# Optimization experiments

Hardware: AMD Instinct MI355X
Metric: run time of the kernel (lower is better)

The kernel has to match this reference:

```python
import jax, jax.numpy as jnp
import numpy as np

TOP_K = 2


def setup_inputs() -> dict:
    key = jax.random.key(0)
    k_x, k_g, k_w1, k_w2, k_w3 = jax.random.split(key, 5)
    B, S, D, H, E = 2, 512, 1024, 512, 8
    x = jax.random.normal(k_x, (B, S, D), dtype=jnp.float32)
    gate_w = jax.random.normal(k_g, (D, E), dtype=jnp.float32) * (D ** -0.5)
    w1 = jax.random.normal(k_w1, (E, D, H), dtype=jnp.float32) * 0.02  # gate proj
    w2 = jax.random.normal(k_w2, (E, H, D), dtype=jnp.float32) * 0.02  # down proj
    w3 = jax.random.normal(k_w3, (E, D, H), dtype=jnp.float32) * 0.02  # up proj
    return {"x": x, "gate_w": gate_w, "w1": w1, "w2": w2, "w3": w3}


def reference(x, gate_w, w1, w2, w3):
    # Token-choice top-k MoE with grouped SwiGLU experts, no shared expert.
    # Equivalent to torchtune MoE: gather routed tokens, scale by top-k router
    # score, run per-expert FFN, scatter-add back. Since each expert's FFN has
    # no bias (FFN(0) == 0), the dispatch/grouped-GEMM/combine is expressed
    # densely as sum_e FFN_e(scale[:, e] * x), which is mathematically identical.
    B, S, D = x.shape
    E = gate_w.shape[1]
    xf = x.reshape(B * S, D)                      # [T, D]
    T = B * S

    logits = xf @ gate_w                          # [T, E]
    scores = jax.nn.softmax(logits, axis=-1)
    top_scores, top_idx = jax.lax.top_k(scores, TOP_K)  # [T, k]

    # scale[t, e] = router score if expert e selected for token t, else 0
    scale = jnp.zeros((T, E), dtype=x.dtype).at[
        jnp.arange(T)[:, None], top_idx
    ].set(top_scores)

    xs = scale.T[:, :, None] * xf[None, :, :]     # [E, T, D] scaled routed input
    h = jax.nn.silu(jnp.einsum('etd,edh->eth', xs, w1)) \
        * jnp.einsum('etd,edh->eth', xs, w3)      # [E, T, H]
    y = jnp.einsum('eth,ehd->etd', h, w2)         # [E, T, D]
    out = y.sum(axis=0)                           # combine (scatter-add equiv)
    return out.reshape(B, S, D)
```

## Files before the change

### kernel.cpp

```cpp
#include <hip/hip_runtime.h>
#include <hip/hip_bf16.h>
#include <cstddef>

#define T_TOK 1024
#define D_DIM 1024
#define H_DIM 512
#define E_EXP 8
#define P_CAP 2560
#define MAX_MT (P_CAP / 64)
#define LDA 72

typedef __attribute__((ext_vector_type(4))) float    float4_t;
typedef __attribute__((ext_vector_type(4))) short    short4_t;
typedef __attribute__((ext_vector_type(8))) short    short8_t;
typedef __attribute__((ext_vector_type(4))) unsigned uint4_t;
typedef __attribute__((ext_vector_type(2))) unsigned uint2_t;

__device__ __forceinline__ short f2bf(float f) {
  union { float f; unsigned u; } v; v.f = f;
  unsigned u = v.u;
  u += 0x7FFFu + ((u >> 16) & 1u);
  return (short)(u >> 16);
}

__device__ __forceinline__ unsigned pkbf(float a, float b) {
  union { __hip_bfloat162 h; unsigned u; } v;
  v.h = __float22bfloat162_rn(make_float2(a, b));
  return v.u;
}

__global__ __launch_bounds__(256) void wconv_kernel(
    const float* __restrict__ src, short* __restrict__ dst,
    int K, int N, int ld_dst, int row_off, size_t src_es, size_t dst_es) {
  __shared__ float tile[64][68];
  const int e  = blockIdx.z;
  const int k0 = blockIdx.x * 64;
  const int n0 = blockIdx.y * 64;
  const int tid = threadIdx.x;
  const float* s = src + (size_t)e * src_es;
  const int kr = tid >> 4, nc = (tid & 15) * 4;
  #pragma unroll
  for (int p = 0; p < 4; ++p) {
    int k = p * 16 + kr;
    float4_t v = *(const float4_t*)(s + (size_t)(k0 + k) * N + n0 + nc);
    *(float4_t*)&tile[k][nc] = v;
  }
  __syncthreads();
  const int r8 = tid >> 3, c8 = tid & 7;
  short* d = dst + (size_t)e * dst_es;
  #pragma unroll
  for (int p = 0; p < 2; ++p) {
    int row = p * 32 + r8;
    uint4_t u;
    #pragma unroll
    for (int j = 0; j < 4; ++j)
      u[j] = pkbf(tile[c8 * 8 + 2 * j][row], tile[c8 * 8 + 2 * j + 1][row]);
    *(uint4_t*)(d + (size_t)(row_off + n0 + row) * ld_dst + k0 + c8 * 8) = u;
  }
}

__global__ __launch_bounds__(256) void router_kernel(
    const float* __restrict__ x, const float* __restrict__ gw,
    int* __restrict__ idx2, float* __restrict__ scale2) {
  const int wid  = threadIdx.x >> 6;
  const int lane = threadIdx.x & 63;
  const int t = blockIdx.x * 4 + wid;
  const float* xr = x + (size_t)t * D_DIM;
  float acc[E_EXP];
  #pragma unroll
  for (int e = 0; e < E_EXP; ++e) acc[e] = 0.f;
  for (int d = lane; d < D_DIM; d += 64) {
    float xv = xr[d];
    float4_t g0 = *(const float4_t*)(gw + d * E_EXP);
    float4_t g1 = *(const float4_t*)(gw + d * E_EXP + 4);
    acc[0] += xv * g0[0]; acc[1] += xv * g0[1];
    acc[2] += xv * g0[2]; acc[3] += xv * g0[3];
    acc[4] += xv * g1[0]; acc[5] += xv * g1[1];
    acc[6] += xv * g1[2]; acc[7] += xv * g1[3];
  }
  #pragma unroll
  for (int off = 32; off >= 1; off >>= 1) {
    #pragma unroll
    for (int e = 0; e < E_EXP; ++e) acc[e] += __shfl_down(acc[e], off, 64);
  }
  if (lane == 0) {
    float m = acc[0];
    #pragma unroll
    for (int e = 1; e < E_EXP; ++e) m = fmaxf(m, acc[e]);
    float p[E_EXP]; float s = 0.f;
    #pragma unroll
    for (int e = 0; e < E_EXP; ++e) { p[e] = __expf(acc[e] - m); s += p[e]; }
    float inv = 1.f / s;
    #pragma unroll
    for (int e = 0; e < E_EXP; ++e) p[e] *= inv;
    int i1 = 0;
    #pragma unroll
    for (int e = 1; e < E_EXP; ++e) if (p[e] > p[i1]) i1 = e;
    int i2 = (i1 == 0) ? 1 : 0;
    #pragma unroll
    for (int e = 0; e < E_EXP; ++e) {
      if (e == i1 || e == i2) continue;
      if (p[e] > p[i2]) i2 = e;
    }
    idx2[2 * t]     = i1;  scale2[2 * t]     = p[i1];
    idx2[2 * t + 1] = i2;  scale2[2 * t + 1] = p[i2];
  }
}

__global__ __launch_bounds__(256) void scan_kernel(
    const int* __restrict__ idx2, const float* __restrict__ scale2,
    int* __restrict__ pair_tok, float* __restrict__ pair_scale,
    int* __restrict__ meta) {
  __shared__ int cnt[E_EXP], base[E_EXP], cur[E_EXP];
  const int tid = threadIdx.x;
  if (tid < E_EXP) { cnt[tid] = 0; cur[tid] = 0; }
  for (int p = tid; p < P_CAP; p += 256) { pair_tok[p] = -1; pair_scale[p] = 0.f; }
  __syncthreads();
  for (int t = tid; t < T_TOK; t += 256) {
    atomicAdd(&cnt[idx2[2 * t]], 1);
    atomicAdd(&cnt[idx2[2 * t + 1]], 1);
  }
  __syncthreads();
  if (tid == 0) {
    int b = 0, g = 0;
    for (int e = 0; e < E_EXP; ++e) {
      base[e] = b;
      int al = (cnt[e] + 63) & ~63;
      for (int j = 0; j < al; j += 64) { meta[1 + g] = e; meta[41 + g] = b + j; ++g; }
      b += al;
    }
    meta[0] = g;
  }
  __syncthreads();
  for (int t = tid; t < T_TOK; t += 256) {
    #pragma unroll
    for (int s = 0; s < 2; ++s) {
      int e = idx2[2 * t + s];
      int p = base[e] + atomicAdd(&cur[e], 1);
      pair_tok[p] = t;
      pair_scale[p] = scale2[2 * t + s];
    }
  }
}

__global__ __launch_bounds__(256, 2) void gemm1_kernel(
    const float* __restrict__ x, const short* __restrict__ w13t,
    const int* __restrict__ pair_tok, const float* __restrict__ pair_scale,
    const int* __restrict__ meta, short* __restrict__ h) {
  __shared__ short As[64 * LDA], B1s[64 * LDA], B3s[64 * LDA];
  const int mt = blockIdx.y;
  if (mt >= meta[0]) return;
  const int e    = meta[1 + mt];
  const int row0 = meta[41 + mt];
  const int n0   = blockIdx.x * 64;
  const int tid = threadIdx.x, lane = tid & 63, wid = tid >> 6;
  const int wr = wid >> 1, wc = wid & 1;
  const int q = lane >> 4, ln = lane & 15;
  const short* bsrc = w13t + (size_t)e * D_DIM * (2 * H_DIM);

  const int ar = tid >> 2, ak = tid & 3;
  const int   tokr = pair_tok[row0 + ar];
  const float sc   = pair_scale[row0 + ar];
  const float* xrow = x + (size_t)(tokr < 0 ? 0 : tokr) * D_DIM + ak * 16;

  const int br = tid >> 3, bu = tid & 7;

  float4_t acc1[2][2], acc3[2][2];
  #pragma unroll
  for (int i = 0; i < 2; ++i)
    #pragma unroll
    for (int j = 0; j < 2; ++j) {
      acc1[i][j] = (float4_t){0.f, 0.f, 0.f, 0.f};
      acc3[i][j] = (float4_t){0.f, 0.f, 0.f, 0.f};
    }

  for (int k0 = 0; k0 < D_DIM; k0 += 64) {
    {
      float4_t v0 = *(const float4_t*)(xrow + k0);
      float4_t v1 = *(const float4_t*)(xrow + k0 + 4);
      float4_t v2 = *(const float4_t*)(xrow + k0 + 8);
      float4_t v3 = *(const float4_t*)(xrow + k0 + 12);
      uint4_t u0 = {pkbf(v0[0] * sc, v0[1] * sc), pkbf(v0[2] * sc, v0[3] * sc),
                    pkbf(v1[0] * sc, v1[1] * sc), pkbf(v1[2] * sc, v1[3] * sc)};
      uint4_t u1 = {pkbf(v2[0] * sc, v2[1] * sc), pkbf(v2[2] * sc, v2[3] * sc),
                    pkbf(v3[0] * sc, v3[1] * sc), pkbf(v3[2] * sc, v3[3] * sc)};
      *(uint4_t*)&As[ar * LDA + ak * 16]     = u0;
      *(uint4_t*)&As[ar * LDA + ak * 16 + 8] = u1;
    }
    #pragma unroll
    for (int p = 0; p < 2; ++p) {
      int row = p * 32 + br;
      uint4_t v1 = *(const uint4_t*)(bsrc + (size_t)(n0 + row) * D_DIM + k0 + bu * 8);
      uint4_t v3 = *(const uint4_t*)(bsrc + (size_t)(H_DIM + n0 + row) * D_DIM + k0 + bu * 8);
      *(uint4_t*)&B1s[row * LDA + bu * 8] = v1;
      *(uint4_t*)&B3s[row * LDA + bu * 8] = v3;
    }
    __syncthreads();

    short8_t af[2][2], b1f[2][2], b3f[2][2];
    #pragma unroll
    for (int i = 0; i < 2; ++i)
      #pragma unroll
      for (int kk = 0; kk < 2; ++kk)
        af[i][kk] = *(const short8_t*)&As[(wr * 32 + i * 16 + ln) * LDA + kk * 32 + q * 8];
    #pragma unroll
    for (int j = 0; j < 2; ++j)
      #pragma unroll
      for (int kk = 0; kk < 2; ++kk) {
        b1f[j][kk] = *(const short8_t*)&B1s[(wc * 32 + j * 16 + ln) * LDA + kk * 32 + q * 8];
        b3f[j][kk] = *(const short8_t*)&B3s[(wc * 32 + j * 16 + ln) * LDA + kk * 32 + q * 8];
      }
    #pragma unroll
    for (int i = 0; i < 2; ++i)
      #pragma unroll
      for (int j = 0; j < 2; ++j)
        #pragma unroll
        for (int kk = 0; kk < 2; ++kk) {
          acc1[i][j] = __builtin_amdgcn_mfma_f32_16x16x32_bf16(af[i][kk], b1f[j][kk], acc1[i][j], 0, 0, 0);
          acc3[i][j] = __builtin_amdgcn_mfma_f32_16x16x32_bf16(af[i][kk], b3f[j][kk], acc3[i][j], 0, 0, 0);
        }
    __syncthreads();
  }

  #pragma unroll
  for (int i = 0; i < 2; ++i) {
    int r_base = row0 + wr * 32 + i * 16 + q * 4;
    #pragma unroll
    for (int j = 0; j < 2; ++j) {
      int col = n0 + wc * 32 + j * 16 + ln;
      #pragma unroll
      for (int rr = 0; rr < 4; ++rr) {
        float c1 = acc1[i][j][rr];
        float c3 = acc3[i][j][rr];
        float sig = 1.f / (1.f + __expf(-c1));
        h[(size_t)(r_base + rr) * H_DIM + col] = f2bf(c1 * sig * c3);
      }
    }
  }
}

__global__ __launch_bounds__(256, 2) void gemm2_kernel(
    const short* __restrict__ h, const short* __restrict__ w2t,
    const int* __restrict__ pair_tok, const int* __restrict__ meta,
    float* __restrict__ out) {
  __shared__ short As[64 * LDA], Bs[64 * LDA];
  const int mt = blockIdx.y;
  if (mt >= meta[0]) return;
  const int e    = meta[1 + mt];
  const int row0 = meta[41 + mt];
  const int n0   = blockIdx.x * 64;
  const int tid = threadIdx.x, lane = tid & 63, wid = tid >> 6;
  const int wr = wid >> 1, wc = wid & 1;
  const int q = lane >> 4, ln = lane & 15;
  const short* bsrc = w2t + (size_t)e * D_DIM * H_DIM;

  const int ar = tid >> 2, ak = tid & 3;
  const short* hrow = h + (size_t)(row0 + ar) * H_DIM + ak * 16;
  const int br = tid >> 3, bu = tid & 7;

  float4_t acc[2][2];
  #pragma unroll
  for (int i = 0; i < 2; ++i)
    #pragma unroll
    for (int j = 0; j < 2; ++j) acc[i][j] = (float4_t){0.f, 0.f, 0.f, 0.f};

  for (int k0 = 0; k0 < H_DIM; k0 += 64) {
    {
      uint4_t u0 = *(const uint4_t*)(hrow + k0);
      uint4_t u1 = *(const uint4_t*)(hrow + k0 + 8);
      *(uint4_t*)&As[ar * LDA + ak * 16]     = u0;
      *(uint4_t*)&As[ar * LDA + ak * 16 + 8] = u1;
    }
    #pragma unroll
    for (int p = 0; p < 2; ++p) {
      int row = p * 32 + br;
      uint4_t v = *(const uint4_t*)(bsrc + (size_t)(n0 + row) * H_DIM + k0 + bu * 8);
      *(uint4_t*)&Bs[row * LDA + bu * 8] = v;
    }
    __syncthreads();

    short8_t af[2][2], bf[2][2];
    #pragma unroll
    for (int i = 0; i < 2; ++i)
      #pragma unroll
      for (int kk = 0; kk < 2; ++kk)
        af[i][kk] = *(const short8_t*)&As[(wr * 32 + i * 16 + ln) * LDA + kk * 32 + q * 8];
    #pragma unroll
    for (int j = 0; j < 2; ++j)
      #pragma unroll
      for (int kk = 0; kk < 2; ++kk)
        bf[j][kk] = *(const short8_t*)&Bs[(wc * 32 + j * 16 + ln) * LDA + kk * 32 + q * 8];
    #pragma unroll
    for (int i = 0; i < 2; ++i)
      #pragma unroll
      for (int j = 0; j < 2; ++j)
        #pragma unroll
        for (int kk = 0; kk < 2; ++kk)
          acc[i][j] = __builtin_amdgcn_mfma_f32_16x16x32_bf16(af[i][kk], bf[j][kk], acc[i][j], 0, 0, 0);
    __syncthreads();
  }

  #pragma unroll
  for (int i = 0; i < 2; ++i) {
    int r_base = row0 + wr * 32 + i * 16 + q * 4;
    #pragma unroll
    for (int rr = 0; rr < 4; ++rr) {
      int tok = pair_tok[r_base + rr];
      if (tok < 0) continue;
      float* orow = out + (size_t)tok * D_DIM;
      #pragma unroll
      for (int j = 0; j < 2; ++j) {
        int col = n0 + wc * 32 + j * 16 + ln;
        atomicAdd(orow + col, acc[i][j][rr]);
      }
    }
  }
}

extern "C" void kernel_launch(void* const* d_in, const int* in_sizes, int n_in,
                              void* d_out, int out_size, void* d_ws, size_t ws_size,
                              hipStream_t stream) {
  const float* x  = (const float*)d_in[0];
  const float* gw = (const float*)d_in[1];
  const float* w1 = (const float*)d_in[2];
  const float* w2 = (const float*)d_in[3];
  const float* w3 = (const float*)d_in[4];
  float* out = (float*)d_out;

  char* ws = (char*)d_ws;
  int*   idx2    = (int*)  (ws);
  float* scale2  = (float*)(ws + 8192);
  int*   ptok    = (int*)  (ws + 16384);
  float* pscale  = (float*)(ws + 32768);
  int*   meta    = (int*)  (ws + 49152);
  short* h       = (short*)(ws + 65536);
  short* w13t    = (short*)(ws + 65536 + (size_t)P_CAP * H_DIM * 2);
  short* w2t     = w13t + (size_t)E_EXP * D_DIM * 2 * H_DIM;

  wconv_kernel<<<dim3(16, 8, E_EXP), dim3(256), 0, stream>>>(
      w1, w13t, D_DIM, H_DIM, D_DIM, 0,     (size_t)D_DIM * H_DIM, (size_t)D_DIM * 2 * H_DIM);
  wconv_kernel<<<dim3(16, 8, E_EXP), dim3(256), 0, stream>>>(
      w3, w13t, D_DIM, H_DIM, D_DIM, H_DIM, (size_t)D_DIM * H_DIM, (size_t)D_DIM * 2 * H_DIM);
  wconv_kernel<<<dim3(8, 16, E_EXP), dim3(256), 0, stream>>>(
      w2, w2t, H_DIM, D_DIM, H_DIM, 0,      (size_t)H_DIM * D_DIM, (size_t)D_DIM * H_DIM);

  router_kernel<<<dim3(T_TOK / 4), dim3(256), 0, stream>>>(x, gw, idx2, scale2);
  scan_kernel<<<dim3(1), dim3(256), 0, stream>>>(idx2, scale2, ptok, pscale, meta);

  gemm1_kernel<<<dim3(H_DIM / 64, MAX_MT), dim3(256), 0, stream>>>(
      x, w13t, ptok, pscale, meta, h);

  hipMemsetAsync(out, 0, (size_t)T_TOK * D_DIM * sizeof(float), stream);
  gemm2_kernel<<<dim3(D_DIM / 64, MAX_MT), dim3(256), 0, stream>>>(
      h, w2t, ptok, meta, out);
}
```

Measured before the change: 158.3 us.

## Double-buffer GEMM tiles, pre-convert routed inputs, merge weight conversion launches

Both expert GEMMs now use register-staged double-buffered shared-memory tiles, so global loads for the next K step overlap the MFMA work on the current one. A new xsconv kernel gathers, scales and converts routed tokens to bf16 once, so gemm1 no longer converts fp32 per tile. Gemm1's N tile is halved to 32 to launch more blocks. The three weight-conversion launches are merged into one grid, and the workspace layout is reorganised. The cost is an extra kernel plus a bf16 xs buffer write and read, and more shared memory per block.

```diff
diff --git a/kernel.cpp b/kernel.cpp
--- a/kernel.cpp
+++ b/kernel.cpp
@@ -11,10 +11,8 @@
 #define LDA 72
 
 typedef __attribute__((ext_vector_type(4))) float    float4_t;
-typedef __attribute__((ext_vector_type(4))) short    short4_t;
 typedef __attribute__((ext_vector_type(8))) short    short8_t;
 typedef __attribute__((ext_vector_type(4))) unsigned uint4_t;
-typedef __attribute__((ext_vector_type(2))) unsigned uint2_t;
 
 __device__ __forceinline__ short f2bf(float f) {
   union { float f; unsigned u; } v; v.f = f;
@@ -30,24 +28,36 @@
 }
 
 __global__ __launch_bounds__(256) void wconv_kernel(
-    const float* __restrict__ src, short* __restrict__ dst,
-    int K, int N, int ld_dst, int row_off, size_t src_es, size_t dst_es) {
+    const float* __restrict__ w1, const float* __restrict__ w3,
+    const float* __restrict__ w2, short* __restrict__ w13t,
+    short* __restrict__ w2t) {
   __shared__ float tile[64][68];
-  const int e  = blockIdx.z;
-  const int k0 = blockIdx.x * 64;
-  const int n0 = blockIdx.y * 64;
+  const int z = blockIdx.z;
+  const float* src; short* dst; int N, ldd, row_off; size_t ses, des;
+  if (z < 16) {
+    if (blockIdx.y >= 8) return;
+    int which = z >> 3, e = z & 7;
+    src = (which ? w3 : w1) + (size_t)e * D_DIM * H_DIM;
+    dst = w13t + (size_t)e * D_DIM * (2 * H_DIM);
+    N = H_DIM; ldd = D_DIM; row_off = which ? H_DIM : 0;
+  } else {
+    if (blockIdx.x >= 8) return;
+    int e = z - 16;
+    src = w2 + (size_t)e * H_DIM * D_DIM;
+    dst = w2t + (size_t)e * D_DIM * H_DIM;
+    N = D_DIM; ldd = H_DIM; row_off = 0;
+  }
+  const int k0 = blockIdx.x * 64, n0 = blockIdx.y * 64;
   const int tid = threadIdx.x;
-  const float* s = src + (size_t)e * src_es;
   const int kr = tid >> 4, nc = (tid & 15) * 4;
   #pragma unroll
   for (int p = 0; p < 4; ++p) {
     int k = p * 16 + kr;
-    float4_t v = *(const float4_t*)(s + (size_t)(k0 + k) * N + n0 + nc);
+    float4_t v = *(const float4_t*)(src + (size_t)(k0 + k) * N + n0 + nc);
     *(float4_t*)&tile[k][nc] = v;
   }
   __syncthreads();
   const int r8 = tid >> 3, c8 = tid & 7;
-  short* d = dst + (size_t)e * dst_es;
   #pragma unroll
   for (int p = 0; p < 2; ++p) {
     int row = p * 32 + r8;
@@ -55,7 +65,7 @@
     #pragma unroll
     for (int j = 0; j < 4; ++j)
       u[j] = pkbf(tile[c8 * 8 + 2 * j][row], tile[c8 * 8 + 2 * j + 1][row]);
-    *(uint4_t*)(d + (size_t)(row_off + n0 + row) * ld_dst + k0 + c8 * 8) = u;
+    *(uint4_t*)(dst + (size_t)(row_off + n0 + row) * ldd + k0 + c8 * 8) = u;
   }
 }
 
@@ -143,98 +153,111 @@
   }
 }
 
+__global__ __launch_bounds__(256) void xsconv_kernel(
+    const float* __restrict__ x, const int* __restrict__ pair_tok,
+    const float* __restrict__ pair_scale, short* __restrict__ xs) {
+  const int row = blockIdx.x * 8 + (threadIdx.x >> 5);
+  const int seg = (threadIdx.x & 31) * 32;
+  const int tok = pair_tok[row];
+  const float sc = pair_scale[row];
+  const float* src = x + (size_t)(tok < 0 ? 0 : tok) * D_DIM + seg;
+  short* dst = xs + (size_t)row * D_DIM + seg;
+  #pragma unroll
+  for (int p = 0; p < 2; ++p) {
+    float4_t v0 = *(const float4_t*)(src + p * 16);
+    float4_t v1 = *(const float4_t*)(src + p * 16 + 4);
+    float4_t v2 = *(const float4_t*)(src + p * 16 + 8);
+    float4_t v3 = *(const float4_t*)(src + p * 16 + 12);
+    uint4_t u0 = {pkbf(v0[0] * sc, v0[1] * sc), pkbf(v0[2] * sc, v0[3] * sc),
+                  pkbf(v1[0] * sc, v1[1] * sc), pkbf(v1[2] * sc, v1[3] * sc)};
+    uint4_t u1 = {pkbf(v2[0] * sc, v2[1] * sc), pkbf(v2[2] * sc, v2[3] * sc),
+                  pkbf(v3[0] * sc, v3[1] * sc), pkbf(v3[2] * sc, v3[3] * sc)};
+    *(uint4_t*)(dst + p * 16)     = u0;
+    *(uint4_t*)(dst + p * 16 + 8) = u1;
+  }
+}
+
 __global__ __launch_bounds__(256, 2) void gemm1_kernel(
-    const float* __restrict__ x, const short* __restrict__ w13t,
-    const int* __restrict__ pair_tok, const float* __restrict__ pair_scale,
+    const short* __restrict__ xs, const short* __restrict__ w13t,
     const int* __restrict__ meta, short* __restrict__ h) {
-  __shared__ short As[64 * LDA], B1s[64 * LDA], B3s[64 * LDA];
+  __shared__ short As[2][64 * LDA];
+  __shared__ short B1s[2][32 * LDA];
+  __shared__ short B3s[2][32 * LDA];
   const int mt = blockIdx.y;
   if (mt >= meta[0]) return;
   const int e    = meta[1 + mt];
   const int row0 = meta[41 + mt];
-  const int n0   = blockIdx.x * 64;
+  const int n0   = blockIdx.x * 32;
   const int tid = threadIdx.x, lane = tid & 63, wid = tid >> 6;
   const int wr = wid >> 1, wc = wid & 1;
   const int q = lane >> 4, ln = lane & 15;
   const short* bsrc = w13t + (size_t)e * D_DIM * (2 * H_DIM);
 
-  const int ar = tid >> 2, ak = tid & 3;
-  const int   tokr = pair_tok[row0 + ar];
-  const float sc   = pair_scale[row0 + ar];
-  const float* xrow = x + (size_t)(tokr < 0 ? 0 : tokr) * D_DIM + ak * 16;
-
-  const int br = tid >> 3, bu = tid & 7;
-
-  float4_t acc1[2][2], acc3[2][2];
-  #pragma unroll
-  for (int i = 0; i < 2; ++i)
-    #pragma unroll
-    for (int j = 0; j < 2; ++j) {
-      acc1[i][j] = (float4_t){0.f, 0.f, 0.f, 0.f};
-      acc3[i][j] = (float4_t){0.f, 0.f, 0.f, 0.f};
-    }
-
-  for (int k0 = 0; k0 < D_DIM; k0 += 64) {
-    {
-      float4_t v0 = *(const float4_t*)(xrow + k0);
-      float4_t v1 = *(const float4_t*)(xrow + k0 + 4);
-      float4_t v2 = *(const float4_t*)(xrow + k0 + 8);
-      float4_t v3 = *(const float4_t*)(xrow + k0 + 12);
-      uint4_t u0 = {pkbf(v0[0] * sc, v0[1] * sc), pkbf(v0[2] * sc, v0[3] * sc),
-                    pkbf(v1[0] * sc, v1[1] * sc), pkbf(v1[2] * sc, v1[3] * sc)};
-      uint4_t u1 = {pkbf(v2[0] * sc, v2[1] * sc), pkbf(v2[2] * sc, v2[3] * sc),
-                    pkbf(v3[0] * sc, v3[1] * sc), pkbf(v3[2] * sc, v3[3] * sc)};
-      *(uint4_t*)&As[ar * LDA + ak * 16]     = u0;
-      *(uint4_t*)&As[ar * LDA + ak * 16 + 8] = u1;
-    }
-    #pragma unroll
-    for (int p = 0; p < 2; ++p) {
-      int row = p * 32 + br;
-      uint4_t v1 = *(const uint4_t*)(bsrc + (size_t)(n0 + row) * D_DIM + k0 + bu * 8);
-      uint4_t v3 = *(const uint4_t*)(bsrc + (size_t)(H_DIM + n0 + row) * D_DIM + k0 + bu * 8);
-      *(uint4_t*)&B1s[row * LDA + bu * 8] = v1;
-      *(uint4_t*)&B3s[row * LDA + bu * 8] = v3;
-    }
-    __syncthreads();
-
-    short8_t af[2][2], b1f[2][2], b3f[2][2];
+  const int ar = tid >> 2, ak = (tid & 3) * 16;
+  const short* arow = xs + (size_t)(row0 + ar) * D_DIM + ak;
+  const int br = tid >> 3, bu = (tid & 7) * 8;
+  const short* b1p = bsrc + (size_t)(n0 + br) * D_DIM + bu;
+  const short* b3p = bsrc + (size_t)(H_DIM + n0 + br) * D_DIM + bu;
+
+  float4_t acc1[2], acc3[2];
+  acc1[0] = acc1[1] = acc3[0] = acc3[1] = (float4_t){0.f, 0.f, 0.f, 0.f};
+
+  uint4_t va0 = *(const uint4_t*)(arow);
+  uint4_t va1 = *(const uint4_t*)(arow + 8);
+  uint4_t vb1 = *(const uint4_t*)(b1p);
+  uint4_t vb3 = *(const uint4_t*)(b3p);
+  *(uint4_t*)&As [0][ar * LDA + ak] = va0;
+  *(uint4_t*)&As [0][ar * LDA + ak + 8] = va1;
+  *(uint4_t*)&B1s[0][br * LDA + bu] = vb1;
+  *(uint4_t*)&B3s[0][br * LDA + bu] = vb3;
+  __syncthreads();
+
+  for (int k = 0; k < 16; ++k) {
+    const int cur = k & 1, nxt = cur ^ 1;
+    if (k < 15) {
+      int k0 = (k + 1) * 64;
+      va0 = *(const uint4_t*)(arow + k0);
+      va1 = *(const uint4_t*)(arow + k0 + 8);
+      vb1 = *(const uint4_t*)(b1p + k0);
+      vb3 = *(const uint4_t*)(b3p + k0);
+    }
+    short8_t af[2][2], b1f[2], b3f[2];
     #pragma unroll
     for (int i = 0; i < 2; ++i)
       #pragma unroll
       for (int kk = 0; kk < 2; ++kk)
-        af[i][kk] = *(const short8_t*)&As[(wr * 32 + i * 16 + ln) * LDA + kk * 32 + q * 8];
-    #pragma unroll
-    for (int j = 0; j < 2; ++j)
+        af[i][kk] = *(const short8_t*)&As[cur][(wr * 32 + i * 16 + ln) * LDA + kk * 32 + q * 8];
+    #pragma unroll
+    for (int kk = 0; kk < 2; ++kk) {
+      b1f[kk] = *(const short8_t*)&B1s[cur][(wc * 16 + ln) * LDA + kk * 32 + q * 8];
+      b3f[kk] = *(const short8_t*)&B3s[cur][(wc * 16 + ln) * LDA + kk * 32 + q * 8];
+    }
+    #pragma unroll
+    for (int i = 0; i < 2; ++i)
       #pragma unroll
       for (int kk = 0; kk < 2; ++kk) {
-        b1f[j][kk] = *(const short8_t*)&B1s[(wc * 32 + j * 16 + ln) * LDA + kk * 32 + q * 8];
-        b3f[j][kk] = *(const short8_t*)&B3s[(wc * 32 + j * 16 + ln) * LDA + kk * 32 + q * 8];
+        acc1[i] = __builtin_amdgcn_mfma_f32_16x16x32_bf16(af[i][kk], b1f[kk], acc1[i], 0, 0, 0);
+        acc3[i] = __builtin_amdgcn_mfma_f32_16x16x32_bf16(af[i][kk], b3f[kk], acc3[i], 0, 0, 0);
       }
-    #pragma unroll
-    for (int i = 0; i < 2; ++i)
-      #pragma unroll
-      for (int j = 0; j < 2; ++j)
-        #pragma unroll
-        for (int kk = 0; kk < 2; ++kk) {
-          acc1[i][j] = __builtin_amdgcn_mfma_f32_16x16x32_bf16(af[i][kk], b1f[j][kk], acc1[i][j], 0, 0, 0);
-          acc3[i][j] = __builtin_amdgcn_mfma_f32_16x16x32_bf16(af[i][kk], b3f[j][kk], acc3[i][j], 0, 0, 0);
-        }
+    if (k < 15) {
+      *(uint4_t*)&As [nxt][ar * LDA + ak] = va0;
+      *(uint4_t*)&As [nxt][ar * LDA + ak + 8] = va1;
+      *(uint4_t*)&B1s[nxt][br * LDA + bu] = vb1;
+      *(uint4_t*)&B3s[nxt][br * LDA + bu] = vb3;
+    }
     __syncthreads();
   }
 
   #pragma unroll
   for (int i = 0; i < 2; ++i) {
     int r_base = row0 + wr * 32 + i * 16 + q * 4;
-    #pragma unroll
-    for (int j = 0; j < 2; ++j) {
-      int col = n0 + wc * 32 + j * 16 + ln;
-      #pragma unroll
-      for (int rr = 0; rr < 4; ++rr) {
-        float c1 = acc1[i][j][rr];
-        float c3 = acc3[i][j][rr];
-        float sig = 1.f / (1.f + __expf(-c1));
-        h[(size_t)(r_base + rr) * H_DIM + col] = f2bf(c1 * sig * c3);
-      }
+    int col = n0 + wc * 16 + ln;
+    #pragma unroll
+    for (int rr = 0; rr < 4; ++rr) {
+      float c1 = acc1[i][rr];
+      float c3 = acc3[i][rr];
+      float sig = 1.f / (1.f + __expf(-c1));
+      h[(size_t)(r_base + rr) * H_DIM + col] = f2bf(c1 * sig * c3);
     }
   }
 }
@@ -243,7 +266,8 @@
     const short* __restrict__ h, const short* __restrict__ w2t,
     const int* __restrict__ pair_tok, const int* __restrict__ meta,
     float* __restrict__ out) {
-  __shared__ short As[64 * LDA], Bs[64 * LDA];
+  __shared__ short As[2][64 * LDA];
+  __shared__ short Bs[2][64 * LDA];
   const int mt = blockIdx.y;
   if (mt >= meta[0]) return;
   const int e    = meta[1 + mt];
@@ -254,9 +278,9 @@
   const int q = lane >> 4, ln = lane & 15;
   const short* bsrc = w2t + (size_t)e * D_DIM * H_DIM;
 
-  const int ar = tid >> 2, ak = tid & 3;
-  const short* hrow = h + (size_t)(row0 + ar) * H_DIM + ak * 16;
-  const int br = tid >> 3, bu = tid & 7;
+  const int ar = tid >> 2, ak = (tid & 3) * 16;
+  const short* arow = h + (size_t)(row0 + ar) * H_DIM + ak;
+  const short* brow = bsrc + (size_t)(n0 + ar) * H_DIM + ak;
 
   float4_t acc[2][2];
   #pragma unroll
@@ -264,32 +288,33 @@
     #pragma unroll
     for (int j = 0; j < 2; ++j) acc[i][j] = (float4_t){0.f, 0.f, 0.f, 0.f};
 
-  for (int k0 = 0; k0 < H_DIM; k0 += 64) {
-    {
-      uint4_t u0 = *(const uint4_t*)(hrow + k0);
-      uint4_t u1 = *(const uint4_t*)(hrow + k0 + 8);
-      *(uint4_t*)&As[ar * LDA + ak * 16]     = u0;
-      *(uint4_t*)&As[ar * LDA + ak * 16 + 8] = u1;
-    }
-    #pragma unroll
-    for (int p = 0; p < 2; ++p) {
-      int row = p * 32 + br;
-      uint4_t v = *(const uint4_t*)(bsrc + (size_t)(n0 + row) * H_DIM + k0 + bu * 8);
-      *(uint4_t*)&Bs[row * LDA + bu * 8] = v;
-    }
-    __syncthreads();
-
+  uint4_t va0 = *(const uint4_t*)(arow);
+  uint4_t va1 = *(const uint4_t*)(arow + 8);
+  uint4_t vb0 = *(const uint4_t*)(brow);
+  uint4_t vb1 = *(const uint4_t*)(brow + 8);
+  *(uint4_t*)&As[0][ar * LDA + ak] = va0;
+  *(uint4_t*)&As[0][ar * LDA + ak + 8] = va1;
+  *(uint4_t*)&Bs[0][ar * LDA + ak] = vb0;
+  *(uint4_t*)&Bs[0][ar * LDA + ak + 8] = vb1;
+  __syncthreads();
+
+  for (int k = 0; k < 8; ++k) {
+    const int cur = k & 1, nxt = cur ^ 1;
+    if (k < 7) {
+      int k0 = (k + 1) * 64;
+      va0 = *(const uint4_t*)(arow + k0);
+      va1 = *(const uint4_t*)(arow + k0 + 8);
+      vb0 = *(const uint4_t*)(brow + k0);
+      vb1 = *(const uint4_t*)(brow + k0 + 8);
+    }
     short8_t af[2][2], bf[2][2];
     #pragma unroll
     for (int i = 0; i < 2; ++i)
       #pragma unroll
-      for (int kk = 0; kk < 2; ++kk)
-        af[i][kk] = *(const short8_t*)&As[(wr * 32 + i * 16 + ln) * LDA + kk * 32 + q * 8];
-    #pragma unroll
-    for (int j = 0; j < 2; ++j)
-      #pragma unroll
-      for (int kk = 0; kk < 2; ++kk)
-        bf[j][kk] = *(const short8_t*)&Bs[(wc * 32 + j * 16 + ln) * LDA + kk * 32 + q * 8];
+      for (int kk = 0; kk < 2; ++kk) {
+        af[i][kk] = *(const short8_t*)&As[cur][(wr * 32 + i * 16 + ln) * LDA + kk * 32 + q * 8];
+        bf[i][kk] = *(const short8_t*)&Bs[cur][(wc * 32 + i * 16 + ln) * LDA + kk * 32 + q * 8];
+      }
     #pragma unroll
     for (int i = 0; i < 2; ++i)
       #pragma unroll
@@ -297,6 +322,12 @@
         #pragma unroll
         for (int kk = 0; kk < 2; ++kk)
           acc[i][j] = __builtin_amdgcn_mfma_f32_16x16x32_bf16(af[i][kk], bf[j][kk], acc[i][j], 0, 0, 0);
+    if (k < 7) {
+      *(uint4_t*)&As[nxt][ar * LDA + ak] = va0;
+      *(uint4_t*)&As[nxt][ar * LDA + ak + 8] = va1;
+      *(uint4_t*)&Bs[nxt][ar * LDA + ak] = vb0;
+      *(uint4_t*)&Bs[nxt][ar * LDA + ak + 8] = vb1;
+    }
     __syncthreads();
   }
 
@@ -333,24 +364,18 @@
   int*   ptok    = (int*)  (ws + 16384);
   float* pscale  = (float*)(ws + 32768);
   int*   meta    = (int*)  (ws + 49152);
-  short* h       = (short*)(ws + 65536);
-  short* w13t    = (short*)(ws + 65536 + (size_t)P_CAP * H_DIM * 2);
-  short* w2t     = w13t + (size_t)E_EXP * D_DIM * 2 * H_DIM;
-
-  wconv_kernel<<<dim3(16, 8, E_EXP), dim3(256), 0, stream>>>(
-      w1, w13t, D_DIM, H_DIM, D_DIM, 0,     (size_t)D_DIM * H_DIM, (size_t)D_DIM * 2 * H_DIM);
-  wconv_kernel<<<dim3(16, 8, E_EXP), dim3(256), 0, stream>>>(
-      w3, w13t, D_DIM, H_DIM, D_DIM, H_DIM, (size_t)D_DIM * H_DIM, (size_t)D_DIM * 2 * H_DIM);
-  wconv_kernel<<<dim3(8, 16, E_EXP), dim3(256), 0, stream>>>(
-      w2, w2t, H_DIM, D_DIM, H_DIM, 0,      (size_t)H_DIM * D_DIM, (size_t)D_DIM * H_DIM);
-
+  short* xs      = (short*)(ws + (1 << 16));
+  short* h       = (short*)(ws + (6u << 20));
+  short* w13t    = (short*)(ws + (9u << 20));
+  short* w2t     = (short*)(ws + (26u << 20));
+
+  wconv_kernel<<<dim3(16, 16, 24), dim3(256), 0, stream>>>(w1, w3, w2, w13t, w2t);
   router_kernel<<<dim3(T_TOK / 4), dim3(256), 0, stream>>>(x, gw, idx2, scale2);
   scan_kernel<<<dim3(1), dim3(256), 0, stream>>>(idx2, scale2, ptok, pscale, meta);
-
-  gemm1_kernel<<<dim3(H_DIM / 64, MAX_MT), dim3(256), 0, stream>>>(
-      x, w13t, ptok, pscale, meta, h);
+  xsconv_kernel<<<dim3(P_CAP / 8), dim3(256), 0, stream>>>(x, ptok, pscale, xs);
+
+  gemm1_kernel<<<dim3(H_DIM / 32, MAX_MT), dim3(256), 0, stream>>>(xs, w13t, meta, h);
 
   hipMemsetAsync(out, 0, (size_t)T_TOK * D_DIM * sizeof(float), stream);
-  gemm2_kernel<<<dim3(D_DIM / 64, MAX_MT), dim3(256), 0, stream>>>(
-      h, w2t, ptok, meta, out);
-}
+  gemm2_kernel<<<dim3(D_DIM / 64, MAX_MT), dim3(256), 0, stream>>>(h, w2t, ptok, meta, out);
+}
```

Result: faster. 152.0 us (-4.0%).
